# Optimization experiments

Hardware: AMD Instinct MI355X
Metric: run time of the kernel (lower is better)

## Reference

```python
import jax, jax.numpy as jnp
import numpy as np


def setup_inputs() -> dict:
    key = jax.random.key(0)
    ks = jax.random.split(key, 8)
    B, Te, De, Dd, H = 64, 1024, 1024, 1024, 1024
    return {
        "encoder_outputs": jax.random.normal(ks[0], (B, Te, De), jnp.float32),
        "decoder_outputs": jax.random.normal(ks[1], (B, 1, Dd), jnp.float32),
        "Wa_w": jax.random.normal(ks[2], (H, Dd), jnp.float32) * 0.02,
        "Wa_b": jax.random.normal(ks[3], (H,), jnp.float32) * 0.02,
        "Ua_w": jax.random.normal(ks[4], (H, De), jnp.float32) * 0.02,
        "Ua_b": jax.random.normal(ks[5], (H,), jnp.float32) * 0.02,
        "Va_w": jax.random.normal(ks[6], (1, H), jnp.float32) * 0.02,
        "Va_b": jax.random.normal(ks[7], (1,), jnp.float32) * 0.02,
    }


def reference(encoder_outputs, decoder_outputs, Wa_w, Wa_b, Ua_w, Ua_b, Va_w, Va_b):
    # Wa: [B,1,H], Ua: [B,Te,H]  (torch Linear: x @ W.T + b)
    Wa = jnp.einsum('bqd,hd->bqh', decoder_outputs, Wa_w) + Wa_b
    Ua = jnp.einsum('bed,hd->beh', encoder_outputs, Ua_w) + Ua_b
    # broadcast add -> tanh -> scalar score per encoder position: [B,Te,1]
    scores = jnp.einsum('beh,oh->beo', jnp.tanh(Wa + Ua), Va_w) + Va_b
    scores = jnp.transpose(scores, (0, 2, 1))          # [B,1,Te]
    weights = jax.nn.softmax(scores, axis=-1)          # softmax over Te
    context = jnp.einsum('bqe,bed->bqd', weights, encoder_outputs)  # [B,1,De]
    return context
```

## Files before the change

kernel.cpp:

```cpp
#include <hip/hip_runtime.h>
#include <hip/hip_bf16.h>

#define B_  64
#define TE  1024
#define K_  1024
#define HH  1024
#define MM  (B_ * TE)

typedef __bf16 bf16x8 __attribute__((ext_vector_type(8)));
typedef __bf16 bf16x4 __attribute__((ext_vector_type(4)));
typedef float  f32x4  __attribute__((ext_vector_type(4)));

__device__ __forceinline__ float fast_tanh(float x) {
    float ax = __builtin_fabsf(x);
    float t  = __expf(-2.0f * ax);
    float r  = (1.0f - t) * __builtin_amdgcn_rcpf(1.0f + t);
    return __builtin_copysignf(r, x);
}

__global__ __launch_bounds__(256) void prep_kernel(const float* __restrict__ Ua_w,
                                                   __bf16* __restrict__ uawB,
                                                   const float* __restrict__ dec,
                                                   const float* __restrict__ Wa_w,
                                                   const float* __restrict__ Wa_b,
                                                   float* __restrict__ WaOut,
                                                   float* __restrict__ scores) {
    int bid = blockIdx.x, tid = threadIdx.x;
    if (bid < 256) {
        long zi = (long)bid * 256 + tid;
        if (zi < MM / 4) ((f32x4*)scores)[zi] = f32x4{0.f, 0.f, 0.f, 0.f};
        const long n4 = (long)HH * 1024 / 4;
        const float4* in4 = (const float4*)Ua_w;
        bf16x4* out4 = (bf16x4*)uawB;
        for (long j = bid * 256 + tid; j < n4; j += 65536) {
            float4 v = in4[j];
            bf16x4 o;
            o[0] = (__bf16)v.x; o[1] = (__bf16)v.y; o[2] = (__bf16)v.z; o[3] = (__bf16)v.w;
            out4[j] = o;
        }
        return;
    }
    int wb = bid - 256;
    int b = wb >> 4, hc = wb & 15;
    int wave = tid >> 6, lane = tid & 63;

    const float4* d4 = (const float4*)(dec + b * 1024);
    float4 dreg[4];
    #pragma unroll
    for (int j = 0; j < 4; j++) dreg[j] = d4[lane * 4 + j];

    #pragma unroll 4
    for (int i = 0; i < 16; i++) {
        int h = hc * 64 + wave * 16 + i;
        const float4* wr = (const float4*)(Wa_w + (long)h * 1024);
        float a = 0.0f;
        #pragma unroll
        for (int j = 0; j < 4; j++) {
            float4 v = wr[lane * 4 + j];
            a += v.x * dreg[j].x + v.y * dreg[j].y + v.z * dreg[j].z + v.w * dreg[j].w;
        }
        #pragma unroll
        for (int off = 32; off > 0; off >>= 1)
            a += __shfl_xor(a, off, 64);
        if (lane == 0) WaOut[b * 1024 + h] = a + Wa_b[h];
    }
}

#define MT 128
#define NP 256
#define KT 64

__global__ __launch_bounds__(256, 2) void score_gemm(
    const float* __restrict__ Af,
    __bf16* __restrict__ encB,
    const __bf16* __restrict__ Bm,
    const float* __restrict__ Wa,
    const float* __restrict__ Ua_b,
    const float* __restrict__ Va_w,
    float* __restrict__ scores)
{
    __shared__ __bf16 sA[MT * KT];
    __shared__ __bf16 sB[NP * KT];
    __shared__ float sVa[NP];
    __shared__ float sWU[NP];

    const int tid  = threadIdx.x;
    const int wave = tid >> 6;
    const int lane = tid & 63;
    const int quad = lane >> 4;
    const int l16  = lane & 15;
    const int wm   = wave >> 1;
    const int wn   = wave & 1;

    const int bid = blockIdx.x;
    const int grp = bid >> 5;
    const int r5  = bid & 31;
    const int y   = r5 >> 3;
    const int x   = grp * 8 + (r5 & 7);

    const int rowBase = x * MT;
    const int colBase = y * NP;
    const int b       = rowBase >> 10;

    if (tid < NP) {
        int h = colBase + tid;
        sVa[tid] = Va_w[h];
        sWU[tid] = Wa[b * 1024 + h] + Ua_b[h];
    }

    int rr[4], sg[4];
    #pragma unroll
    for (int i = 0; i < 4; i++) {
        int c = i * 256 + tid;
        rr[i] = c >> 3;
        sg[i] = (c & 7) ^ (rr[i] & 7);
    }

    f32x4 acc[4][8] = {};

    const long aBase = (long)rowBase * K_;
    const long bBase = (long)colBase * K_;

    float4 pre[4][2];
    #pragma unroll
    for (int i = 0; i < 4; i++) {
        const float4* p = (const float4*)(Af + aBase + (long)rr[i] * K_ + sg[i] * 8);
        pre[i][0] = p[0]; pre[i][1] = p[1];
    }

    for (int k0 = 0; k0 < K_; k0 += KT) {
        const bool wb = (((k0 >> 6) & 3) == y);
        __syncthreads();
        #pragma unroll
        for (int i = 0; i < 4; i++) {
            bf16x8 v;
            v[0] = (__bf16)pre[i][0].x; v[1] = (__bf16)pre[i][0].y;
            v[2] = (__bf16)pre[i][0].z; v[3] = (__bf16)pre[i][0].w;
            v[4] = (__bf16)pre[i][1].x; v[5] = (__bf16)pre[i][1].y;
            v[6] = (__bf16)pre[i][1].z; v[7] = (__bf16)pre[i][1].w;
            *(bf16x8*)(sA + (i * 256 + tid) * 8) = v;
            if (wb)
                *(bf16x8*)(encB + aBase + (long)rr[i] * K_ + k0 + sg[i] * 8) = v;
        }
        #pragma unroll
        for (int i = 0; i < 8; i++) {
            int c = i * 256 + tid;
            int r = c >> 3, slot = c & 7;
            int seg = slot ^ (r & 7);
            __builtin_amdgcn_global_load_lds(
                (const __attribute__((address_space(1))) unsigned int*)(Bm + bBase + (long)r * K_ + k0 + seg * 8),
                (__attribute__((address_space(3))) unsigned int*)(sB + c * 8), 16, 0, 0);
        }
        __syncthreads();

        if (k0 + KT < K_) {
            #pragma unroll
            for (int i = 0; i < 4; i++) {
                const float4* p = (const float4*)(Af + aBase + (long)rr[i] * K_ + (k0 + KT) + sg[i] * 8);
                pre[i][0] = p[0]; pre[i][1] = p[1];
            }
        }

        #pragma unroll
        for (int ks = 0; ks < 2; ks++) {
            bf16x8 bfr[8];
            #pragma unroll
            for (int t = 0; t < 8; t++) {
                int r = wn * 128 + t * 16 + l16;
                int slot = (ks * 4 + quad) ^ (r & 7);
                bfr[t] = *(const bf16x8*)(sB + r * KT + slot * 8);
            }
            #pragma unroll
            for (int s = 0; s < 4; s++) {
                int r = wm * 64 + s * 16 + l16;
                int slot = (ks * 4 + quad) ^ (r & 7);
                bf16x8 af = *(const bf16x8*)(sA + r * KT + slot * 8);
                #pragma unroll
                for (int t = 0; t < 8; t++)
                    acc[s][t] = __builtin_amdgcn_mfma_f32_16x16x32_bf16(af, bfr[t], acc[s][t], 0, 0, 0);
            }
        }
    }

    float rs[4][4] = {};
    #pragma unroll
    for (int s = 0; s < 4; s++)
        #pragma unroll
        for (int t = 0; t < 8; t++) {
            int hl = wn * 128 + t * 16 + l16;
            float va = sVa[hl], wu = sWU[hl];
            #pragma unroll
            for (int r = 0; r < 4; r++)
                rs[s][r] += va * fast_tanh(acc[s][t][r] + wu);
        }

    #pragma unroll
    for (int s = 0; s < 4; s++)
        #pragma unroll
        for (int r = 0; r < 4; r++) {
            float v = rs[s][r];
            v += __shfl_xor(v, 1, 64);
            v += __shfl_xor(v, 2, 64);
            v += __shfl_xor(v, 4, 64);
            v += __shfl_xor(v, 8, 64);
            if (l16 == 0)
                atomicAdd(&scores[rowBase + wm * 64 + s * 16 + quad * 4 + r], v);
        }
}

__global__ __launch_bounds__(256) void context_partial(const __bf16* __restrict__ enc,
                                                       const float* __restrict__ sc,
                                                       float* __restrict__ pb) {
    __shared__ float red[2][128][8];
    __shared__ float wLds[128];
    __shared__ float xr[8];
    int b = blockIdx.x, ec = blockIdx.y, tid = threadIdx.x;
    int wave = tid >> 6, lane = tid & 63;

    float4 v = ((const float4*)(sc + b * 1024))[tid];
    float m = fmaxf(fmaxf(v.x, v.y), fmaxf(v.z, v.w));
    #pragma unroll
    for (int off = 32; off > 0; off >>= 1)
        m = fmaxf(m, __shfl_xor(m, off, 64));
    if (lane == 0) xr[wave] = m;
    __syncthreads();
    m = fmaxf(fmaxf(xr[0], xr[1]), fmaxf(xr[2], xr[3]));
    float ex = expf(v.x - m), ey = expf(v.y - m), ez = expf(v.z - m), ew = expf(v.w - m);
    float sum = ex + ey + ez + ew;
    #pragma unroll
    for (int off = 32; off > 0; off >>= 1)
        sum += __shfl_xor(sum, off, 64);
    if (lane == 0) xr[4 + wave] = sum;
    __syncthreads();
    float inv = 1.0f / (xr[4] + xr[5] + xr[6] + xr[7]);
    int u = tid - ec * 32;
    if (u >= 0 && u < 32) {
        wLds[u * 4 + 0] = ex * inv;
        wLds[u * 4 + 1] = ey * inv;
        wLds[u * 4 + 2] = ez * inv;
        wLds[u * 4 + 3] = ew * inv;
    }
    __syncthreads();

    int eo = tid >> 7;
    int dc = tid & 127;
    const bf16x8* enc8 = (const bf16x8*)(enc + ((long)b * 1024 + ec * 128) * 1024);
    float acc[8] = {};
    #pragma unroll 4
    for (int e = eo; e < 128; e += 2) {
        float we = wLds[e];
        bf16x8 vv = enc8[e * 128 + dc];
        #pragma unroll
        for (int j = 0; j < 8; j++) acc[j] += we * (float)vv[j];
    }
    #pragma unroll
    for (int j = 0; j < 8; j++) red[eo][dc][j] = acc[j];
    __syncthreads();
    if (eo == 0) {
        float* o = pb + ((long)(b * 8 + ec)) * 1024 + dc * 8;
        #pragma unroll
        for (int j = 0; j < 8; j++) o[j] = red[0][dc][j] + red[1][dc][j];
    }
}

__global__ void context_reduce(const float* __restrict__ pb, float* __restrict__ out) {
    int b = blockIdx.x, tid = threadIdx.x;
    const f32x4* p4 = (const f32x4*)pb;
    f32x4 s = {0.f, 0.f, 0.f, 0.f};
    #pragma unroll
    for (int ec = 0; ec < 8; ec++)
        s += p4[(b * 8 + ec) * 256 + tid];
    ((f32x4*)out)[b * 256 + tid] = s;
}

extern "C" void kernel_launch(void* const* d_in, const int* in_sizes, int n_in,
                              void* d_out, int out_size, void* d_ws, size_t ws_size,
                              hipStream_t stream) {
    (void)in_sizes; (void)n_in; (void)ws_size; (void)out_size;
    const float* enc   = (const float*)d_in[0];
    const float* dec   = (const float*)d_in[1];
    const float* Wa_w  = (const float*)d_in[2];
    const float* Wa_b  = (const float*)d_in[3];
    const float* Ua_w  = (const float*)d_in[4];
    const float* Ua_b  = (const float*)d_in[5];
    const float* Va_w  = (const float*)d_in[6];
    float* out = (float*)d_out;

    char* w = (char*)d_ws;
    __bf16* encB = (__bf16*)w;  w += (size_t)MM * 1024 * 2;
    __bf16* uawB = (__bf16*)w;  w += (size_t)HH * 1024 * 2;
    float* WaBuf = (float*)w;   w += (size_t)B_ * HH * 4;
    float* scores = (float*)w;  w += (size_t)MM * 4;
    float* pb = (float*)w;      w += (size_t)B_ * 8 * 1024 * 4;

    prep_kernel<<<dim3(256 + B_ * 16), 256, 0, stream>>>(Ua_w, uawB, dec, Wa_w, Wa_b, WaBuf, scores);
    score_gemm<<<dim3((MM / MT) * (HH / NP)), 256, 0, stream>>>(enc, encB, uawB, WaBuf, Ua_b, Va_w, scores);
    context_partial<<<dim3(B_, 8), 256, 0, stream>>>(encB, scores, pb);
    context_reduce<<<dim3(B_), 256, 0, stream>>>(pb, out);
}
```

Baseline: 511.0 us.

## Fuse four kernels into one persistent cooperative kernel with grid syncs

Merges prep, score GEMM, context partial and reduce into a single cooperative mega_kernel of 512 blocks that loops over virtual block ids and separates the phases with grid.sync(). The aim is to remove kernel launch gaps and tail effects between stages. The old multi-kernel path stays as a fallback if the cooperative launch fails. In exchange, the score GEMM runs a fixed 512-block persistent grid instead of 2048 hardware-scheduled blocks, and grid-wide barriers add their own cost.

```diff
diff --git a/kernel.cpp b/kernel.cpp
--- a/kernel.cpp
+++ b/kernel.cpp
@@ -1,5 +1,8 @@
 #include <hip/hip_runtime.h>
+#include <hip/hip_cooperative_groups.h>
 #include <hip/hip_bf16.h>
+
+namespace cg = cooperative_groups;
 
 #define B_  64
 #define TE  1024
@@ -18,21 +21,21 @@
     return __builtin_copysignf(r, x);
 }
 
-__global__ __launch_bounds__(256) void prep_kernel(const float* __restrict__ Ua_w,
-                                                   __bf16* __restrict__ uawB,
-                                                   const float* __restrict__ dec,
-                                                   const float* __restrict__ Wa_w,
-                                                   const float* __restrict__ Wa_b,
-                                                   float* __restrict__ WaOut,
-                                                   float* __restrict__ scores) {
-    int bid = blockIdx.x, tid = threadIdx.x;
-    if (bid < 256) {
-        long zi = (long)bid * 256 + tid;
+__device__ __forceinline__ void prep_body(int vb, int tid,
+                                          const float* __restrict__ Ua_w,
+                                          __bf16* __restrict__ uawB,
+                                          const float* __restrict__ dec,
+                                          const float* __restrict__ Wa_w,
+                                          const float* __restrict__ Wa_b,
+                                          float* __restrict__ WaOut,
+                                          float* __restrict__ scores) {
+    if (vb < 256) {
+        long zi = (long)vb * 256 + tid;
         if (zi < MM / 4) ((f32x4*)scores)[zi] = f32x4{0.f, 0.f, 0.f, 0.f};
         const long n4 = (long)HH * 1024 / 4;
         const float4* in4 = (const float4*)Ua_w;
         bf16x4* out4 = (bf16x4*)uawB;
-        for (long j = bid * 256 + tid; j < n4; j += 65536) {
+        for (long j = vb * 256 + tid; j < n4; j += 65536) {
             float4 v = in4[j];
             bf16x4 o;
             o[0] = (__bf16)v.x; o[1] = (__bf16)v.y; o[2] = (__bf16)v.z; o[3] = (__bf16)v.w;
@@ -40,7 +43,7 @@
         }
         return;
     }
-    int wb = bid - 256;
+    int wb = vb - 256;
     int b = wb >> 4, hc = wb & 15;
     int wave = tid >> 6, lane = tid & 63;
 
@@ -70,21 +73,18 @@
 #define NP 256
 #define KT 64
 
-__global__ __launch_bounds__(256, 2) void score_gemm(
-    const float* __restrict__ Af,
-    __bf16* __restrict__ encB,
-    const __bf16* __restrict__ Bm,
-    const float* __restrict__ Wa,
-    const float* __restrict__ Ua_b,
-    const float* __restrict__ Va_w,
+__device__ __forceinline__ void score_tile_body(
+    int vt, int tid, char* smemRaw,
+    const float* __restrict__ Af, __bf16* __restrict__ encB,
+    const __bf16* __restrict__ Bm, const float* __restrict__ Wa,
+    const float* __restrict__ Ua_b, const float* __restrict__ Va_w,
     float* __restrict__ scores)
 {
-    __shared__ __bf16 sA[MT * KT];
-    __shared__ __bf16 sB[NP * KT];
-    __shared__ float sVa[NP];
-    __shared__ float sWU[NP];
-
-    const int tid  = threadIdx.x;
+    __bf16* sA = (__bf16*)smemRaw;
+    __bf16* sB = (__bf16*)(smemRaw + 16384);
+    float* sVa = (float*)(smemRaw + 49152);
+    float* sWU = (float*)(smemRaw + 50176);
+
     const int wave = tid >> 6;
     const int lane = tid & 63;
     const int quad = lane >> 4;
@@ -92,9 +92,8 @@
     const int wm   = wave >> 1;
     const int wn   = wave & 1;
 
-    const int bid = blockIdx.x;
-    const int grp = bid >> 5;
-    const int r5  = bid & 31;
+    const int grp = vt >> 5;
+    const int r5  = vt & 31;
     const int y   = r5 >> 3;
     const int x   = grp * 8 + (r5 & 7);
 
@@ -102,6 +101,7 @@
     const int colBase = y * NP;
     const int b       = rowBase >> 10;
 
+    __syncthreads();
     if (tid < NP) {
         int h = colBase + tid;
         sVa[tid] = Va_w[h];
@@ -208,13 +208,14 @@
         }
 }
 
-__global__ __launch_bounds__(256) void context_partial(const __bf16* __restrict__ enc,
-                                                       const float* __restrict__ sc,
-                                                       float* __restrict__ pb) {
-    __shared__ float red[2][128][8];
-    __shared__ float wLds[128];
-    __shared__ float xr[8];
-    int b = blockIdx.x, ec = blockIdx.y, tid = threadIdx.x;
+__device__ __forceinline__ void context_body(int vb, int tid, char* smemRaw,
+                                             const __bf16* __restrict__ enc,
+                                             const float* __restrict__ sc,
+                                             float* __restrict__ pb) {
+    float (*red)[128][8] = (float (*)[128][8])smemRaw;
+    float* wLds = (float*)(smemRaw + 8192);
+    float* xr   = (float*)(smemRaw + 8704);
+    int b = vb >> 3, ec = vb & 7;
     int wave = tid >> 6, lane = tid & 63;
 
     float4 v = ((const float4*)(sc + b * 1024))[tid];
@@ -263,14 +264,72 @@
     }
 }
 
-__global__ void context_reduce(const float* __restrict__ pb, float* __restrict__ out) {
-    int b = blockIdx.x, tid = threadIdx.x;
+__device__ __forceinline__ void reduce_body(int b, int tid,
+                                            const float* __restrict__ pb,
+                                            float* __restrict__ out) {
     const f32x4* p4 = (const f32x4*)pb;
     f32x4 s = {0.f, 0.f, 0.f, 0.f};
     #pragma unroll
     for (int ec = 0; ec < 8; ec++)
         s += p4[(b * 8 + ec) * 256 + tid];
     ((f32x4*)out)[b * 256 + tid] = s;
+}
+
+__global__ __launch_bounds__(256, 2) void mega_kernel(
+    const float* __restrict__ enc, __bf16* __restrict__ encB,
+    __bf16* __restrict__ uawB, const float* __restrict__ dec,
+    const float* __restrict__ Wa_w, const float* __restrict__ Wa_b,
+    const float* __restrict__ Ua_w, const float* __restrict__ Ua_b,
+    const float* __restrict__ Va_w, float* __restrict__ WaBuf,
+    float* __restrict__ scores, float* __restrict__ pb,
+    float* __restrict__ out)
+{
+    cg::grid_group grid = cg::this_grid();
+    __shared__ __align__(16) char smemRaw[51200];
+    const int tid = threadIdx.x, bid0 = blockIdx.x;
+
+    for (int vb = bid0; vb < 1280; vb += 512)
+        prep_body(vb, tid, Ua_w, uawB, dec, Wa_w, Wa_b, WaBuf, scores);
+    grid.sync();
+
+    for (int vt = bid0; vt < 2048; vt += 512)
+        score_tile_body(vt, tid, smemRaw, enc, encB, uawB, WaBuf, Ua_b, Va_w, scores);
+    grid.sync();
+
+    context_body(bid0, tid, smemRaw, encB, scores, pb);
+    grid.sync();
+
+    if (bid0 < 64) reduce_body(bid0, tid, pb, out);
+}
+
+__global__ __launch_bounds__(256) void prep_kernel(const float* __restrict__ Ua_w,
+                                                   __bf16* __restrict__ uawB,
+                                                   const float* __restrict__ dec,
+                                                   const float* __restrict__ Wa_w,
+                                                   const float* __restrict__ Wa_b,
+                                                   float* __restrict__ WaOut,
+                                                   float* __restrict__ scores) {
+    prep_body(blockIdx.x, threadIdx.x, Ua_w, uawB, dec, Wa_w, Wa_b, WaOut, scores);
+}
+
+__global__ __launch_bounds__(256, 2) void score_gemm(
+    const float* __restrict__ Af, __bf16* __restrict__ encB,
+    const __bf16* __restrict__ Bm, const float* __restrict__ Wa,
+    const float* __restrict__ Ua_b, const float* __restrict__ Va_w,
+    float* __restrict__ scores) {
+    __shared__ __align__(16) char smemRaw[51200];
+    score_tile_body(blockIdx.x, threadIdx.x, smemRaw, Af, encB, Bm, Wa, Ua_b, Va_w, scores);
+}
+
+__global__ __launch_bounds__(256) void context_partial(const __bf16* __restrict__ enc,
+                                                       const float* __restrict__ sc,
+                                                       float* __restrict__ pb) {
+    __shared__ __align__(16) char smemRaw[8736];
+    context_body(blockIdx.x * 8 + blockIdx.y, threadIdx.x, smemRaw, enc, sc, pb);
+}
+
+__global__ void context_reduce(const float* __restrict__ pb, float* __restrict__ out) {
+    reduce_body(blockIdx.x, threadIdx.x, pb, out);
 }
 
 extern "C" void kernel_launch(void* const* d_in, const int* in_sizes, int n_in,
@@ -293,8 +352,16 @@
     float* scores = (float*)w;  w += (size_t)MM * 4;
     float* pb = (float*)w;      w += (size_t)B_ * 8 * 1024 * 4;
 
-    prep_kernel<<<dim3(256 + B_ * 16), 256, 0, stream>>>(Ua_w, uawB, dec, Wa_w, Wa_b, WaBuf, scores);
-    score_gemm<<<dim3((MM / MT) * (HH / NP)), 256, 0, stream>>>(enc, encB, uawB, WaBuf, Ua_b, Va_w, scores);
-    context_partial<<<dim3(B_, 8), 256, 0, stream>>>(encB, scores, pb);
-    context_reduce<<<dim3(B_), 256, 0, stream>>>(pb, out);
-}
+    void* args[] = {(void*)&enc, (void*)&encB, (void*)&uawB, (void*)&dec,
+                    (void*)&Wa_w, (void*)&Wa_b, (void*)&Ua_w, (void*)&Ua_b,
+                    (void*)&Va_w, (void*)&WaBuf, (void*)&scores, (void*)&pb,
+                    (void*)&out};
+    hipError_t err = hipLaunchCooperativeKernel((void*)mega_kernel, dim3(512), dim3(256),
+                                                args, 0, stream);
+    if (err != hipSuccess) {
+        prep_kernel<<<dim3(256 + B_ * 16), 256, 0, stream>>>(Ua_w, uawB, dec, Wa_w, Wa_b, WaBuf, scores);
+        score_gemm<<<dim3((MM / MT) * (HH / NP)), 256, 0, stream>>>(enc, encB, uawB, WaBuf, Ua_b, Va_w, scores);
+        context_partial<<<dim3(B_, 8), 256, 0, stream>>>(encB, scores, pb);
+        context_reduce<<<dim3(B_), 256, 0, stream>>>(pb, out);
+    }
+}
```

Result: slower. 734.4 us (+43.7%).
